# Kernel optimization log

Measured on AMD Instinct MI355X. Metric: run time of the kernel, lower is better.

The kernel has to match this reference:

```python
import jax, jax.numpy as jnp
import numpy as np

N = 100000      # num_entities
D = 128         # embedding_dim
H = 128         # hidden_layer_size
R2 = 100        # num_relations * 2 (with inverse relations)
B = 4           # num_bases
E = 400000      # num_edges


def setup_inputs() -> dict:
    key = jax.random.key(0)
    ks = jax.random.split(key, 12)
    s = 0.1
    return {
        "edge_index": jax.random.randint(ks[0], (2, E), 0, N),
        "edge_type": jax.random.randint(ks[1], (E,), 0, R2),
        "entity_embedding": jax.random.normal(ks[2], (N, D), jnp.float32) * s,
        "entity_embedding_bias": jnp.zeros((1, D), jnp.float32),
        "bases1": jax.random.normal(ks[3], (B, D, H), jnp.float32) * s,
        "comp1": jax.random.normal(ks[4], (R2, B), jnp.float32) * s,
        "root1": jax.random.normal(ks[5], (D, H), jnp.float32) * s,
        "bias1": jnp.zeros((H,), jnp.float32),
        "bases2": jax.random.normal(ks[6], (B, H, D), jnp.float32) * s,
        "comp2": jax.random.normal(ks[7], (R2, B), jnp.float32) * s,
        "root2": jax.random.normal(ks[8], (H, D), jnp.float32) * s,
        "bias2": jnp.zeros((D,), jnp.float32),
        "rel_emb": jax.random.normal(ks[9], (R2, D), jnp.float32) * s,
    }


def _rgcn_layer(x, bases, comp, root, bias, src, dst, et, norm):
    # gather source features and project through all bases: [E, B, out]
    xb = jnp.einsum('ei,bio->ebo', x[src], bases)
    # relation-specific basis mix per edge: [E, out]
    msg = jnp.einsum('eb,ebo->eo', comp[et], xb) * norm[:, None]
    # scatter-add aggregate to destination nodes
    agg = jax.ops.segment_sum(msg, dst, num_segments=N)
    return agg + x @ root + bias


def reference(edge_index, edge_type, entity_embedding, entity_embedding_bias,
              bases1, comp1, root1, bias1, bases2, comp2, root2, bias2, rel_emb):
    src, dst = edge_index[0], edge_index[1]
    # schlichtkrull normalization: 1 / |{edges into dst with same relation}|
    key = dst * R2 + edge_type
    counts = jax.ops.segment_sum(jnp.ones((E,), jnp.float32), key, num_segments=N * R2)
    norm = 1.0 / jnp.maximum(counts[key], 1.0)

    x = jax.nn.relu(entity_embedding + entity_embedding_bias)
    x = _rgcn_layer(x, bases1, comp1, root1, bias1, src, dst, edge_type, norm)
    x = jax.nn.relu(x)
    x = _rgcn_layer(x, bases2, comp2, root2, bias2, src, dst, edge_type, norm)

    # DistMult decoder over triples (src, edge_type, dst)
    score = jnp.sum(x[src] * rel_emb[edge_type] * x[dst], axis=-1)  # [E]
    # L2 penalty on relation embeddings
    penalty = jnp.sum(rel_emb ** 2)
    return score, penalty
```

## Files before the change

kernel.cpp:

```cpp
#include <hip/hip_runtime.h>

#define N_NODES 100000
#define DIM     128
#define RR      100
#define NE      400000
#define NBLK    196
#define NPB     32

typedef float  floatx4 __attribute__((ext_vector_type(4)));
typedef float  floatx2 __attribute__((ext_vector_type(2)));
typedef __bf16 bf16x8  __attribute__((ext_vector_type(8)));

static __device__ __forceinline__ unsigned short f2b(float f) {
    union { float f; unsigned int i; } v; v.f = f;
    unsigned int u = v.i;
    unsigned int r = (u + 0x7fffu + ((u >> 16) & 1u)) >> 16;
    return (unsigned short)r;
}
static __device__ __forceinline__ float b2f(unsigned int u16) {
    union { unsigned int i; float f; } v; v.i = u16 << 16; return v.f;
}
static __device__ __forceinline__ unsigned packbf(float a, float b) {
    return (unsigned)f2b(a) | ((unsigned)f2b(b) << 16);
}

__global__ void k_deg(const int* __restrict__ dst, int* __restrict__ deg, int E) {
    int e = blockIdx.x * 256 + threadIdx.x;
    if (e < E) atomicAdd(&deg[dst[e]], 1);
}

__global__ void k_scan_block(const int* __restrict__ deg, int* __restrict__ bsum) {
    __shared__ int sm[256];
    int b = blockIdx.x, t = threadIdx.x;
    int i0 = b * 512 + 2 * t;
    int a = (i0     < N_NODES) ? deg[i0]     : 0;
    int c = (i0 + 1 < N_NODES) ? deg[i0 + 1] : 0;
    sm[t] = a + c;
    __syncthreads();
    for (int s = 128; s > 0; s >>= 1) { if (t < s) sm[t] += sm[t + s]; __syncthreads(); }
    if (t == 0) bsum[b] = sm[0];
}

__global__ void k_scan_top(const int* __restrict__ bsum, int* __restrict__ boff) {
    __shared__ int sm[256];
    int t = threadIdx.x;
    int v = (t < NBLK) ? bsum[t] : 0;
    sm[t] = v;
    __syncthreads();
    for (int s = 1; s < 256; s <<= 1) {
        int u = (t >= s) ? sm[t - s] : 0;
        __syncthreads();
        sm[t] += u;
        __syncthreads();
    }
    if (t < NBLK) boff[t] = sm[t] - v;
}

__global__ void k_scan_down(const int* __restrict__ deg, const int* __restrict__ boff,
                            int* __restrict__ off) {
    __shared__ int sm[256];
    int b = blockIdx.x, t = threadIdx.x;
    int i0 = b * 512 + 2 * t;
    int a = (i0     < N_NODES) ? deg[i0]     : 0;
    int c = (i0 + 1 < N_NODES) ? deg[i0 + 1] : 0;
    int ts = a + c;
    sm[t] = ts;
    __syncthreads();
    for (int s = 1; s < 256; s <<= 1) {
        int u = (t >= s) ? sm[t - s] : 0;
        __syncthreads();
        sm[t] += u;
        __syncthreads();
    }
    int base = boff[b] + (sm[t] - ts);
    if (i0     < N_NODES) off[i0]     = base;
    if (i0 + 1 < N_NODES) off[i0 + 1] = base + a;
    if (b == 0 && t == 0) off[N_NODES] = NE;
}

__global__ void k_scatter(const int* __restrict__ src, const int* __restrict__ dst,
                          const int* __restrict__ et, const int* __restrict__ off,
                          int* __restrict__ cursor, int4* __restrict__ edesc, int E) {
    int e = blockIdx.x * 256 + threadIdx.x;
    if (e >= E) return;
    int d = dst[e];
    int pos = off[d] + atomicAdd(&cursor[d], 1);
    edesc[pos] = make_int4(src[e], (et[e] << 19) | e, d, 0);
}

__global__ void k_norm2(const int* __restrict__ off, int4* __restrict__ edesc, int E) {
    int p = blockIdx.x * 256 + threadIdx.x;
    if (p >= E) return;
    int4 me = edesc[p];
    int myt = me.y >> 19;
    int p0 = off[me.z], p1 = off[me.z + 1];
    int c = 0;
    for (int j = p0; j < p1; ++j)
        c += ((((const int*)edesc)[4 * j + 1] >> 19) == myt) ? 1 : 0;
    ((int*)edesc)[4 * p + 3] = __float_as_int(1.0f / (float)c);
}

__global__ void k_pre(const float* __restrict__ ent, const float* __restrict__ entb,
                      const float* __restrict__ bases1, const float* __restrict__ root1,
                      const float* __restrict__ bases2, const float* __restrict__ root2,
                      const float* __restrict__ rel,
                      unsigned short* __restrict__ x1,
                      unsigned short* __restrict__ wt1, unsigned short* __restrict__ wt2,
                      unsigned short* __restrict__ relb, float* __restrict__ out,
                      int* __restrict__ deg, int* __restrict__ cursor) {
    int b = blockIdx.x, t = threadIdx.x;
    if (b < 50000) {
        int i = b * 256 + t;
        float v = ent[i] + entb[i & (DIM - 1)];
        x1[i] = f2b(v > 0.0f ? v : 0.0f);
    } else if (b < 50320) {
        int i = (b - 50000) * 256 + t;
        int m = i / 640, k = i - m * 640;
        float v1, v2;
        if (k < 512) {
            int bb = k >> 7, kin = k & 127;
            v1 = bases1[(bb * 128 + kin) * 128 + m];
            v2 = bases2[(bb * 128 + kin) * 128 + m];
        } else {
            int kin = k - 512;
            v1 = root1[kin * 128 + m];
            v2 = root2[kin * 128 + m];
        }
        int o = (k >> 5) * 4096 + m * 32 + (k & 31);
        wt1[o] = f2b(v1);
        wt2[o] = f2b(v2);
    } else if (b < 50370) {
        int i = (b - 50320) * 256 + t;
        relb[i] = f2b(rel[i]);
    } else if (b < 51152) {
        int j = (b - 50370) * 256 + t;
        if (j < N_NODES) deg[j] = 0;
        else if (j < 2 * N_NODES) cursor[j - N_NODES] = 0;
    } else {
        __shared__ float sm[256];
        float v = 0.0f;
        for (int i = t; i < RR * DIM; i += 256) { float x = rel[i]; v += x * x; }
        sm[t] = v;
        __syncthreads();
        for (int s = 128; s > 0; s >>= 1) {
            if (t < s) sm[t] += sm[t + s];
            __syncthreads();
        }
        if (t == 0) out[NE] = sm[0];
    }
}

#define ACC(A) { A[0] += (floatx2){w0, w0} * xv; \
                 A[1] += (floatx2){w1, w1} * xv; \
                 A[2] += (floatx2){w2, w2} * xv; \
                 A[3] += (floatx2){w3, w3} * xv; }

__global__ __launch_bounds__(512, 4) void k_fused(const unsigned short* __restrict__ X,
                                                  const int4* __restrict__ edesc,
                                                  const int* __restrict__ off,
                                                  const float* __restrict__ comp,
                                                  const unsigned short* __restrict__ WT,
                                                  const float* __restrict__ bias,
                                                  unsigned short* __restrict__ out,
                                                  int do_relu) {
    __shared__ __align__(16) unsigned short Sacc[4 * NPB * 128];
    __shared__ float4 Cs[RR];

    const int t = threadIdx.x, wid = t >> 6, lane = t & 63;
    const int rbase = blockIdx.x * NPB;

    if (t < RR) Cs[t] = ((const float4*)comp)[t];
    __syncthreads();

    {
        const int nbase = rbase + wid * 4;
        const int lo = off[nbase], hi = off[nbase + 4];
        floatx2 a0[4], a1[4], a2[4], a3[4];
#pragma unroll
        for (int c = 0; c < 4; ++c) {
            a0[c] = (floatx2)0.0f; a1[c] = (floatx2)0.0f;
            a2[c] = (floatx2)0.0f; a3[c] = (floatx2)0.0f;
        }
        for (int base = lo; base < hi; base += 16) {
            int cnt = hi - base; if (cnt > 16) cnt = 16;
            int4 md = edesc[base + (lane & 15)];
            unsigned xp[16];
#pragma unroll
            for (int u = 0; u < 16; ++u) {
                int jc = (u < cnt) ? u : 0;
                int s = (int)__builtin_amdgcn_readlane((unsigned)md.x, (unsigned)jc);
                xp[u] = *(const unsigned*)(X + (size_t)s * 128 + 2 * lane);
            }
#pragma unroll
            for (int u = 0; u < 16; ++u) {
                if (u < cnt) {
                    int row = (int)__builtin_amdgcn_readlane((unsigned)md.z, (unsigned)u) - nbase;
                    int tt  = (int)__builtin_amdgcn_readlane((unsigned)md.y, (unsigned)u) >> 19;
                    float w = __int_as_float(__builtin_amdgcn_readlane((unsigned)md.w, (unsigned)u));
                    float4 cc = Cs[tt];
                    floatx2 xv = {b2f(xp[u] & 0xffffu), b2f(xp[u] >> 16)};
                    float w0 = w * cc.x, w1 = w * cc.y, w2 = w * cc.z, w3 = w * cc.w;
                    if      (row == 0) ACC(a0)
                    else if (row == 1) ACC(a1)
                    else if (row == 2) ACC(a2)
                    else               ACC(a3)
                }
            }
        }
        const int sw16 = lane >> 2, wo = 2 * (lane & 3);
#pragma unroll
        for (int r = 0; r < 4; ++r) {
            int R = wid * 4 + r;
            unsigned bo = (unsigned)(R * 128 + ((sw16 ^ (R & 15)) << 3) + wo);
            floatx2* A = (r == 0) ? a0 : (r == 1) ? a1 : (r == 2) ? a2 : a3;
#pragma unroll
            for (int c = 0; c < 4; ++c)
                *(unsigned*)(Sacc + c * (NPB * 128) + bo) = packbf(A[c].x, A[c].y);
        }
    }

    const int quad = lane >> 4, lr = lane & 15;
    const int wr = wid & 1, wc = wid >> 1;

    bf16x8 ax[4];
    {
        int grow = rbase + wr * 16 + lr;
#pragma unroll
        for (int ks = 0; ks < 4; ++ks)
            ax[ks] = *(const bf16x8*)(X + (size_t)grow * 128 + ks * 32 + quad * 8);
    }

    floatx4 acc[2];
    acc[0] = (floatx4)0.0f; acc[1] = (floatx4)0.0f;

    __syncthreads();

    const unsigned short* wbase = WT + (wc * 32 + lr) * 32 + quad * 8;

#pragma unroll
    for (int kc = 0; kc < 5; ++kc) {
#pragma unroll
        for (int ks = 0; ks < 4; ++ks) {
            bf16x8 a, b0, b1;
            int R = wr * 16 + lr;
            if (kc < 4) {
                int ch = ((ks * 4 + quad) ^ (R & 15)) << 3;
                a = *(const bf16x8*)(Sacc + kc * (NPB * 128) + R * 128 + ch);
            } else {
                a = ax[ks];
            }
            const unsigned short* wseg = wbase + (kc * 4 + ks) * 4096;
            b0 = *(const bf16x8*)(wseg);
            b1 = *(const bf16x8*)(wseg + 16 * 32);
            acc[0] = __builtin_amdgcn_mfma_f32_16x16x32_bf16(a, b0, acc[0], 0, 0, 0);
            acc[1] = __builtin_amdgcn_mfma_f32_16x16x32_bf16(a, b1, acc[1], 0, 0, 0);
        }
    }

#pragma unroll
    for (int reg = 0; reg < 4; ++reg) {
        int R = wr * 16 + quad * 4 + reg;
        int grow = rbase + R;
#pragma unroll
        for (int nj = 0; nj < 2; ++nj) {
            int n = wc * 32 + nj * 16 + lr;
            float v = acc[nj][reg] + bias[n];
            if (do_relu) v = v > 0.0f ? v : 0.0f;
            out[(size_t)grow * 128 + n] = f2b(v);
        }
    }
}

__global__ __launch_bounds__(256) void k_score(const unsigned short* __restrict__ xf,
                                               const int* __restrict__ src, const int* __restrict__ dst,
                                               const int* __restrict__ et,
                                               const unsigned short* __restrict__ relb,
                                               float* __restrict__ out, int E) {
    int g = threadIdx.x >> 4, li = threadIdx.x & 15;
    int e = blockIdx.x * 16 + g;
    if (e >= E) return;
    int s = src[e], d = dst[e], tt = et[e];
    uint4 au = *(const uint4*)(xf + (size_t)s * 128 + li * 8);
    uint4 bu = *(const uint4*)(xf + (size_t)d * 128 + li * 8);
    uint4 ru = *(const uint4*)(relb + (size_t)tt * 128 + li * 8);
    float v;
    v  = b2f(au.x & 0xffffu) * b2f(ru.x & 0xffffu) * b2f(bu.x & 0xffffu);
    v += b2f(au.x >> 16)     * b2f(ru.x >> 16)     * b2f(bu.x >> 16);
    v += b2f(au.y & 0xffffu) * b2f(ru.y & 0xffffu) * b2f(bu.y & 0xffffu);
    v += b2f(au.y >> 16)     * b2f(ru.y >> 16)     * b2f(bu.y >> 16);
    v += b2f(au.z & 0xffffu) * b2f(ru.z & 0xffffu) * b2f(bu.z & 0xffffu);
    v += b2f(au.z >> 16)     * b2f(ru.z >> 16)     * b2f(bu.z >> 16);
    v += b2f(au.w & 0xffffu) * b2f(ru.w & 0xffffu) * b2f(bu.w & 0xffffu);
    v += b2f(au.w >> 16)     * b2f(ru.w >> 16)     * b2f(bu.w >> 16);
    v += __shfl_xor(v, 8, 16);
    v += __shfl_xor(v, 4, 16);
    v += __shfl_xor(v, 2, 16);
    v += __shfl_xor(v, 1, 16);
    if (li == 0) out[e] = v;
}

extern "C" void kernel_launch(void* const* d_in, const int* in_sizes, int n_in,
                              void* d_out, int out_size, void* d_ws, size_t ws_size,
                              hipStream_t stream) {
    (void)in_sizes; (void)n_in; (void)out_size; (void)ws_size;
    const int* edge_index = (const int*)d_in[0];
    const int* edge_type  = (const int*)d_in[1];
    const float* ent    = (const float*)d_in[2];
    const float* entb   = (const float*)d_in[3];
    const float* bases1 = (const float*)d_in[4];
    const float* comp1  = (const float*)d_in[5];
    const float* root1  = (const float*)d_in[6];
    const float* bias1  = (const float*)d_in[7];
    const float* bases2 = (const float*)d_in[8];
    const float* comp2  = (const float*)d_in[9];
    const float* root2  = (const float*)d_in[10];
    const float* bias2  = (const float*)d_in[11];
    const float* rel    = (const float*)d_in[12];
    const int* src = edge_index;
    const int* dst = edge_index + NE;

    char* ws = (char*)d_ws;
    size_t off_b = 0;
    auto alloc = [&](size_t bytes) { void* p = ws + off_b; off_b = (off_b + bytes + 255) & ~(size_t)255; return p; };

    unsigned short* x1   = (unsigned short*)alloc((size_t)N_NODES * 128 * 2);
    unsigned short* x2   = (unsigned short*)alloc((size_t)N_NODES * 128 * 2);
    unsigned short* wt1  = (unsigned short*)alloc(128 * 640 * 2);
    unsigned short* wt2  = (unsigned short*)alloc(128 * 640 * 2);
    unsigned short* relb = (unsigned short*)alloc(RR * DIM * 2);
    int*   deg    = (int*)alloc((size_t)N_NODES * 4);
    int*   cursor = (int*)alloc((size_t)N_NODES * 4);
    int*   offv   = (int*)alloc((size_t)(N_NODES + 1) * 4);
    int*   bsum   = (int*)alloc(NBLK * 4);
    int*   boff   = (int*)alloc(NBLK * 4);
    int4*  edesc  = (int4*)alloc((size_t)(NE + 64) * 16);

    float* out = (float*)d_out;

    k_pre<<<51153, 256, 0, stream>>>(ent, entb, bases1, root1, bases2, root2, rel,
                                     x1, wt1, wt2, relb, out, deg, cursor);
    k_deg<<<(NE + 255) / 256, 256, 0, stream>>>(dst, deg, NE);
    k_scan_block<<<NBLK, 256, 0, stream>>>(deg, bsum);
    k_scan_top<<<1, 256, 0, stream>>>(bsum, boff);
    k_scan_down<<<NBLK, 256, 0, stream>>>(deg, boff, offv);
    k_scatter<<<(NE + 255) / 256, 256, 0, stream>>>(src, dst, edge_type, offv, cursor, edesc, NE);
    k_norm2<<<(NE + 255) / 256, 256, 0, stream>>>(offv, edesc, NE);

    int fgrid = N_NODES / NPB;
    k_fused<<<fgrid, 512, 0, stream>>>(x1, edesc, offv, comp1, wt1, bias1, x2, 1);
    k_fused<<<fgrid, 512, 0, stream>>>(x2, edesc, offv, comp2, wt2, bias2, x1, 0);
    k_score<<<(NE + 15) / 16, 256, 0, stream>>>(x1, src, dst, edge_type, relb, out, NE);
}
```

Before: 434.5 us.

## Stage weight tiles through double-buffered LDS in fused RGCN GEMM

The transformed weight matrix is now stored row-major (128 x 640 bf16) rather than in a pre-tiled layout. In the fused layer kernel, each 32-wide K chunk of weights is loaded cooperatively into a swizzled, double-buffered shared-memory tile, and the next chunk is prefetched while MFMAs run on the current one. Before, each wave read B fragments directly from global memory. The change adds 20 block-wide barriers and 16 KB of LDS per block, which may reduce occupancy, in exchange for coalesced loads that are shared across waves.

```diff
diff --git a/kernel.cpp b/kernel.cpp
--- a/kernel.cpp
+++ b/kernel.cpp
@@ -126,9 +126,8 @@
             v1 = root1[kin * 128 + m];
             v2 = root2[kin * 128 + m];
         }
-        int o = (k >> 5) * 4096 + m * 32 + (k & 31);
-        wt1[o] = f2b(v1);
-        wt2[o] = f2b(v2);
+        wt1[i] = f2b(v1);
+        wt2[i] = f2b(v2);
     } else if (b < 50370) {
         int i = (b - 50320) * 256 + t;
         relb[i] = f2b(rel[i]);
@@ -164,6 +163,8 @@
                                                   unsigned short* __restrict__ out,
                                                   int do_relu) {
     __shared__ __align__(16) unsigned short Sacc[4 * NPB * 128];
+    __shared__ __align__(16) unsigned short Bs0[128 * 32];
+    __shared__ __align__(16) unsigned short Bs1[128 * 32];
     __shared__ float4 Cs[RR];
 
     const int t = threadIdx.x, wid = t >> 6, lane = t & 63;
@@ -222,6 +223,11 @@
     const int quad = lane >> 4, lr = lane & 15;
     const int wr = wid & 1, wc = wid >> 1;
 
+    const int srow = t >> 2, sg = t & 3;
+    const unsigned bo = (unsigned)(srow * 32 + ((sg ^ ((srow >> 1) & 3)) << 3));
+
+    uint4 p0 = *(const uint4*)(WT + (size_t)srow * 640 + sg * 8);
+
     bf16x8 ax[4];
     {
         int grow = rbase + wr * 16 + lr;
@@ -233,34 +239,41 @@
     floatx4 acc[2];
     acc[0] = (floatx4)0.0f; acc[1] = (floatx4)0.0f;
 
-    __syncthreads();
-
-    const unsigned short* wbase = WT + (wc * 32 + lr) * 32 + quad * 8;
-
-#pragma unroll
-    for (int kc = 0; kc < 5; ++kc) {
-#pragma unroll
-        for (int ks = 0; ks < 4; ++ks) {
-            bf16x8 a, b0, b1;
-            int R = wr * 16 + lr;
-            if (kc < 4) {
-                int ch = ((ks * 4 + quad) ^ (R & 15)) << 3;
-                a = *(const bf16x8*)(Sacc + kc * (NPB * 128) + R * 128 + ch);
-            } else {
-                a = ax[ks];
-            }
-            const unsigned short* wseg = wbase + (kc * 4 + ks) * 4096;
-            b0 = *(const bf16x8*)(wseg);
-            b1 = *(const bf16x8*)(wseg + 16 * 32);
-            acc[0] = __builtin_amdgcn_mfma_f32_16x16x32_bf16(a, b0, acc[0], 0, 0, 0);
-            acc[1] = __builtin_amdgcn_mfma_f32_16x16x32_bf16(a, b1, acc[1], 0, 0, 0);
-        }
+    *(uint4*)(Bs0 + bo) = p0;
+    __syncthreads();
+
+    const int R = wr * 16 + lr;
+    const int brow0 = wc * 32 + lr, brow1 = brow0 + 16;
+    const unsigned bq0 = (unsigned)(brow0 * 32 + ((quad ^ ((brow0 >> 1) & 3)) << 3));
+    const unsigned bq1 = (unsigned)(brow1 * 32 + ((quad ^ ((brow1 >> 1) & 3)) << 3));
+
+#pragma unroll
+    for (int c = 0; c < 20; ++c) {
+        const unsigned short* Bcur = (c & 1) ? Bs1 : Bs0;
+        unsigned short*      Bnext = (c & 1) ? Bs0 : Bs1;
+        uint4 nx;
+        if (c < 19)
+            nx = *(const uint4*)(WT + (size_t)srow * 640 + (c + 1) * 32 + sg * 8);
+        bf16x8 a, b0, b1;
+        if (c < 16) {
+            int ch = (((c & 3) * 4 + quad) ^ (R & 15)) << 3;
+            a = *(const bf16x8*)(Sacc + (c >> 2) * (NPB * 128) + R * 128 + ch);
+        } else {
+            a = ax[c - 16];
+        }
+        b0 = *(const bf16x8*)(Bcur + bq0);
+        b1 = *(const bf16x8*)(Bcur + bq1);
+        acc[0] = __builtin_amdgcn_mfma_f32_16x16x32_bf16(a, b0, acc[0], 0, 0, 0);
+        acc[1] = __builtin_amdgcn_mfma_f32_16x16x32_bf16(a, b1, acc[1], 0, 0, 0);
+        if (c < 19)
+            *(uint4*)(Bnext + bo) = nx;
+        __syncthreads();
     }
 
 #pragma unroll
     for (int reg = 0; reg < 4; ++reg) {
-        int R = wr * 16 + quad * 4 + reg;
-        int grow = rbase + R;
+        int Ro = wr * 16 + quad * 4 + reg;
+        int grow = rbase + Ro;
 #pragma unroll
         for (int nj = 0; nj < 2; ++nj) {
             int n = wc * 32 + nj * 16 + lr;
```

Measured after the change: 400.1 us. -7.9%, faster.
